# Optimization experiments

Measured on AMD Instinct MI355X. Metric: run time of the kernel, lower is better.

## Reference

```python
import jax, jax.numpy as jnp
import numpy as np

B, K = 16, 256
APP, DK, DG, NR = 768, 96, 96, 8


def setup_inputs() -> dict:
    key = jax.random.key(0)
    ks = jax.random.split(key, 10)
    sA = 1.0 / np.sqrt(APP)  # torch Linear default init scale
    sG = 1.0 / np.sqrt(DG)
    return {
        "f_a": jax.random.normal(ks[0], (B, K, APP), jnp.float32),
        "position_embedding": jax.random.uniform(ks[1], (B, K, K, DG), jnp.float32),
        "WG_w": jax.random.normal(ks[2], (NR, DG), jnp.float32) * sG,
        "WG_b": jnp.zeros((NR,), jnp.float32),
        "WK_w": jax.random.normal(ks[3], (NR, DK, APP), jnp.float32) * sA,
        "WK_b": jnp.zeros((NR, DK), jnp.float32),
        "WQ_w": jax.random.normal(ks[4], (NR, DK, APP), jnp.float32) * sA,
        "WQ_b": jnp.zeros((NR, DK), jnp.float32),
        "WV_w": jax.random.normal(ks[5], (NR, DK, APP), jnp.float32) * sA,
        "WV_b": jnp.zeros((NR, DK), jnp.float32),
    }


def reference(f_a, position_embedding, WG_w, WG_b, WK_w, WK_b, WQ_w, WQ_b, WV_w, WV_b):
    # geometric bias: [NR, B, K, K]
    w_g = jax.nn.relu(jnp.einsum('bmng,rg->rbmn', position_embedding, WG_w)
                      + WG_b[:, None, None, None])
    # projections: [NR, B, K, DK]
    w_k = jnp.einsum('bmd,rkd->rbmk', f_a, WK_w) + WK_b[:, None, None, :]
    w_q = jnp.einsum('bnd,rkd->rbnk', f_a, WQ_w) + WQ_b[:, None, None, :]
    w_v = jnp.einsum('bmd,rkd->rbmk', f_a, WV_w) + WV_b[:, None, None, :]
    # scaled dot: scores[r,b,m,n] = <k_m, q_n>/sqrt(DK)
    scores = jnp.einsum('rbmk,rbnk->rbmn', w_k, w_q) / jnp.sqrt(jnp.float32(DK))
    logits = jnp.log(jnp.clip(w_g, 1e-6)) + scores
    # softmax over m (the key index, torch dim=1 of [B,K,K])
    att = jax.nn.softmax(logits, axis=2)
    # out[r,b,n,k] = sum_m att[r,b,m,n] * v[r,b,m,k]
    out = jnp.einsum('rbmn,rbmk->rbnk', att, w_v)
    # concat units along feature dim -> [B, K, NR*DK], residual add
    out = out.transpose(1, 2, 0, 3).reshape(B, K, NR * DK)
    return out + f_a
```

## Files before the change

### kernel.cpp

```cpp
#include <hip/hip_runtime.h>
#include <hip/hip_bf16.h>

typedef __attribute__((ext_vector_type(8))) short s16x8;
typedef __attribute__((ext_vector_type(4))) float f32x4;
typedef unsigned short u16;
typedef unsigned int u32;

#define NB 16
#define NK 256
#define APP 768
#define DKK 96
#define NR 8
#define QSCALE 0.10206207261596575f

__device__ __forceinline__ u16 f2bf(float f) {
  union { float f; unsigned int u; } v; v.f = f;
  unsigned int x = v.u;
  x += 0x7fffu + ((x >> 16) & 1u);
  return (u16)(x >> 16);
}
__device__ __forceinline__ float bf2f(u16 h) {
  union { unsigned int u; float f; } v; v.u = ((unsigned int)h) << 16;
  return v.f;
}
__device__ __forceinline__ u32 cvtpk(float lo, float hi) {
  u32 r;
  asm("v_cvt_pk_bf16_f32 %0, %1, %2" : "=v"(r) : "v"(lo), "v"(hi));
  return r;
}
__device__ __forceinline__ float bflo(u32 pk) {
  union { u32 u; float f; } v; v.u = pk << 16; return v.f;
}
__device__ __forceinline__ float bfhi(u32 pk) {
  union { u32 u; float f; } v; v.u = pk & 0xffff0000u; return v.f;
}
__device__ __forceinline__ void gload_lds16(const void* g, void* l) {
  __builtin_amdgcn_global_load_lds(
      (const __attribute__((address_space(1))) unsigned int*)g,
      (__attribute__((address_space(3))) unsigned int*)l, 16, 0, 0);
}

__global__ __launch_bounds__(256) void conv_kernel(
    const float* __restrict__ fa,
    const float* __restrict__ WKw, const float* __restrict__ WQw,
    const float* __restrict__ WVw,
    u16* __restrict__ fab, u16* __restrict__ Wb)
{
  const int idx = blockIdx.x * 256 + threadIdx.x;
  const int faCh = NB * NK * APP / 8;
  const int wCh  = NR * DKK * APP / 8;
  const float* src; u16* dst;
  if (idx < faCh) {
    src = fa + (size_t)idx * 8;
    dst = fab + (size_t)idx * 8;
  } else {
    int o = idx - faCh;
    int a = o / wCh;
    int oo = o - a * wCh;
    const float* wsrc = a == 0 ? WKw : (a == 1 ? WQw : WVw);
    src = wsrc + (size_t)oo * 8;
    dst = Wb + (size_t)a * (NR * DKK * APP) + (size_t)oo * 8;
  }
  float4 v0 = *(const float4*)src;
  float4 v1 = *(const float4*)(src + 4);
  s16x8 ov = {(short)f2bf(v0.x),(short)f2bf(v0.y),(short)f2bf(v0.z),(short)f2bf(v0.w),
              (short)f2bf(v1.x),(short)f2bf(v1.y),(short)f2bf(v1.z),(short)f2bf(v1.w)};
  *(s16x8*)dst = ov;
}

__global__ __launch_bounds__(256) void proj_kernel(
    const u16* __restrict__ fab, const u16* __restrict__ Wb,
    const float* __restrict__ WKb, const float* __restrict__ WQb,
    const float* __restrict__ WVb,
    u16* __restrict__ wkF, u16* __restrict__ wqF, u16* __restrict__ wvF)
{
  __shared__ u16 As[128 * 64];
  __shared__ u16 Bs[128 * 64];
  const int t = threadIdx.x;
  const int lane = t & 63, w = t >> 6;
  const int c = lane & 15, g = lane >> 4;
  const int wr = w >> 1, wc = w & 1;
  const int m0 = blockIdx.x * 128;
  const int ct = blockIdx.y;
  const int c0 = ct * 128;

  f32x4 acc[4][4] = {};

  for (int k0 = 0; k0 < APP; k0 += 64) {
    __syncthreads();
    #pragma unroll
    for (int i = 0; i < 4; ++i) {
      int n = t + i * 256;
      int row = n >> 3, cg = n & 7;
      int scg = cg ^ (row & 7);
      gload_lds16(fab + (size_t)(m0 + row) * APP + k0 + scg * 8, As + n * 8);
      gload_lds16(Wb  + (size_t)(c0 + row) * APP + k0 + scg * 8, Bs + n * 8);
    }
    __syncthreads();
    #pragma unroll
    for (int kc = 0; kc < 2; ++kc) {
      s16x8 af[4], bfr[4];
      #pragma unroll
      for (int i = 0; i < 4; ++i) {
        int arow = wr * 64 + i * 16 + c;
        af[i]  = *(const s16x8*)(As + (((arow << 3) | ((kc * 4 + g) ^ (arow & 7))) << 3));
        int brow = wc * 64 + i * 16 + c;
        bfr[i] = *(const s16x8*)(Bs + (((brow << 3) | ((kc * 4 + g) ^ (brow & 7))) << 3));
      }
      #pragma unroll
      for (int mi = 0; mi < 4; ++mi)
        #pragma unroll
        for (int ni = 0; ni < 4; ++ni)
          acc[mi][ni] = __builtin_amdgcn_mfma_f32_16x16x32_bf16(af[mi], bfr[ni], acc[mi][ni], 0, 0, 0);
    }
  }

  const int arr = ct / 6;
  const int cw0 = c0 - arr * APP;
  const float* bp = arr == 0 ? WKb : (arr == 1 ? WQb : WVb);

  #pragma unroll
  for (int mi = 0; mi < 4; ++mi)
    #pragma unroll
    for (int ni = 0; ni < 4; ++ni) {
      int clw = cw0 + wc * 64 + ni * 16 + c;
      float bias = bp[clw];
      int rr = clw / DKK, kk = clw - rr * DKK;
      int mb = m0 + wr * 64 + mi * 16 + g * 4;
      int bi = mb >> 8, tt = mb & 255;
      size_t hb = (size_t)rr * NB + bi;
      if (arr == 2) {
        ushort4 pk4;
        pk4.x = f2bf(acc[mi][ni][0] + bias);
        pk4.y = f2bf(acc[mi][ni][1] + bias);
        pk4.z = f2bf(acc[mi][ni][2] + bias);
        pk4.w = f2bf(acc[mi][ni][3] + bias);
        *(ushort4*)&wvF[((hb * 32 + (tt >> 3)) * DKK + kk) * 8 + (tt & 7)] = pk4;
      } else {
        u16* op = arr == 0 ? wkF : wqF;
        size_t base = ((hb * 12 + (kk >> 3)) * NK) * 8 + (size_t)(kk & 7);
        #pragma unroll
        for (int e = 0; e < 4; ++e) {
          float val = acc[mi][ni][e] + bias;
          if (arr == 1) val *= QSCALE;
          op[base + (size_t)(tt + e) * 8] = f2bf(val);
        }
      }
    }
}

__global__ __launch_bounds__(256) void wg_kernel(
    const float* __restrict__ pos,
    const float* __restrict__ WGw, const float* __restrict__ WGb,
    u16* __restrict__ lb2)
{
  __shared__ u16 Th[128 * 104];
  __shared__ u16 Tl[128 * 104];
  const int t = threadIdx.x;
  const int lane = t & 63, w = t >> 6;
  const int c = lane & 15, g = lane >> 4;
  const size_t row0 = (size_t)blockIdx.x * 128;

  s16x8 bwh[3], bwl[3];
  #pragma unroll
  for (int kc = 0; kc < 3; ++kc) {
    const float* wp = WGw + (c & 7) * DKK + kc * 32 + g * 8;
    s16x8 hv, lv;
    #pragma unroll
    for (int j = 0; j < 4; ++j) {
      float x0 = wp[2 * j], x1 = wp[2 * j + 1];
      u32 h = cvtpk(x0, x1);
      u32 l = cvtpk(x0 - bflo(h), x1 - bfhi(h));
      hv[2 * j] = (short)(h & 0xffff); hv[2 * j + 1] = (short)(h >> 16);
      lv[2 * j] = (short)(l & 0xffff); lv[2 * j + 1] = (short)(l >> 16);
    }
    bwh[kc] = hv; bwl[kc] = lv;
  }
  const float bias = WGb[c & 7];

  #pragma unroll
  for (int i = 0; i < 6; ++i) {
    int q = t + i * 256;
    int row = q / 12, col8 = q - row * 12;
    const float* s = pos + row0 * DKK + (size_t)q * 8;
    float4 a = *(const float4*)s;
    float4 b = *(const float4*)(s + 4);
    uint4 ph, pl;
    ph.x = cvtpk(a.x, a.y); pl.x = cvtpk(a.x - bflo(ph.x), a.y - bfhi(ph.x));
    ph.y = cvtpk(a.z, a.w); pl.y = cvtpk(a.z - bflo(ph.y), a.w - bfhi(ph.y));
    ph.z = cvtpk(b.x, b.y); pl.z = cvtpk(b.x - bflo(ph.z), b.y - bfhi(ph.z));
    ph.w = cvtpk(b.z, b.w); pl.w = cvtpk(b.z - bflo(ph.w), b.w - bfhi(ph.w));
    *(uint4*)&Th[row * 104 + col8 * 8] = ph;
    *(uint4*)&Tl[row * 104 + col8 * 8] = pl;
  }
  __syncthreads();

  #pragma unroll
  for (int gi = 0; gi < 2; ++gi) {
    int rowl = w * 32 + gi * 16;
    f32x4 acc = {0.f, 0.f, 0.f, 0.f};
    #pragma unroll
    for (int kc = 0; kc < 3; ++kc) {
      s16x8 ah = *(const s16x8*)&Th[(rowl + c) * 104 + kc * 32 + g * 8];
      s16x8 al = *(const s16x8*)&Tl[(rowl + c) * 104 + kc * 32 + g * 8];
      acc = __builtin_amdgcn_mfma_f32_16x16x32_bf16(ah, bwh[kc], acc, 0, 0, 0);
      acc = __builtin_amdgcn_mfma_f32_16x16x32_bf16(ah, bwl[kc], acc, 0, 0, 0);
      acc = __builtin_amdgcn_mfma_f32_16x16x32_bf16(al, bwh[kc], acc, 0, 0, 0);
    }
    if (c < 8) {
      size_t base = (size_t)c * (NB * NK * NK) + row0 + rowl + g * 4;
      #pragma unroll
      for (int e = 0; e < 4; ++e) {
        float v = __logf(fmaxf(acc[e] + bias, 1e-6f));
        lb2[base + e] = f2bf(v);
      }
    }
  }
}

__global__ __launch_bounds__(256) void attn_kernel(
    const u16* __restrict__ wkF, const u16* __restrict__ wqF,
    const u16* __restrict__ wvF, const u16* __restrict__ lb2,
    const float* __restrict__ fa, float* __restrict__ out)
{
  __shared__ u16 Ps[4][16][40];
  const int t = threadIdx.x;
  const int w = t >> 6, lane = t & 63;
  const int c = lane & 15, g = lane >> 4;
  const int b = blockIdx.y, r = blockIdx.z;
  const int nb = blockIdx.x * 64 + w * 16;

  const size_t hb = (size_t)r * NB + b;
  const u16* Qb = wqF + hb * (12 * NK * 8);
  const u16* Kb = wkF + hb * (12 * NK * 8);
  const u16* Vb = wvF + hb * (32 * DKK * 8);
  const u16* Br = lb2 + hb * NK * NK + (size_t)c * NK + nb + g * 4;

  s16x8 qf[3];
  #pragma unroll
  for (int kc = 0; kc < 3; ++kc)
    qf[kc] = *(const s16x8*)(Qb + ((kc * 4 + g) * NK + nb + c) * 8);

  ushort4 bbr[16];
  #pragma unroll
  for (int mt = 0; mt < 16; ++mt)
    bbr[mt] = *(const ushort4*)(Br + (size_t)mt * 16 * NK);

  f32x4 S[16];
  #pragma unroll
  for (int mt = 0; mt < 16; ++mt) {
    f32x4 sa = {bf2f(bbr[mt].x), bf2f(bbr[mt].y), bf2f(bbr[mt].z), bf2f(bbr[mt].w)};
    #pragma unroll
    for (int kc = 0; kc < 3; ++kc) {
      s16x8 kf = *(const s16x8*)(Kb + ((kc * 4 + g) * NK + mt * 16 + c) * 8);
      sa = __builtin_amdgcn_mfma_f32_16x16x32_bf16(qf[kc], kf, sa, 0, 0, 0);
    }
    S[mt] = sa;
  }

  float rinv[4];
  #pragma unroll
  for (int e = 0; e < 4; ++e) {
    float mx = S[0][e];
    #pragma unroll
    for (int mt = 1; mt < 16; ++mt) mx = fmaxf(mx, S[mt][e]);
    mx = fmaxf(mx, __shfl_xor(mx, 1));
    mx = fmaxf(mx, __shfl_xor(mx, 2));
    mx = fmaxf(mx, __shfl_xor(mx, 4));
    mx = fmaxf(mx, __shfl_xor(mx, 8));
    float sm = 0.f;
    #pragma unroll
    for (int mt = 0; mt < 16; ++mt) {
      float p = __expf(S[mt][e] - mx);
      S[mt][e] = p;
      sm += p;
    }
    sm += __shfl_xor(sm, 1);
    sm += __shfl_xor(sm, 2);
    sm += __shfl_xor(sm, 4);
    sm += __shfl_xor(sm, 8);
    rinv[e] = 1.f / sm;
  }

  f32x4 o[6];
  #pragma unroll
  for (int ki = 0; ki < 6; ++ki) o[ki] = (f32x4){0.f, 0.f, 0.f, 0.f};

  #pragma unroll
  for (int mc = 0; mc < 8; ++mc) {
    #pragma unroll
    for (int e = 0; e < 4; ++e) {
      Ps[w][g * 4 + e][c]      = f2bf(S[2 * mc][e]);
      Ps[w][g * 4 + e][16 + c] = f2bf(S[2 * mc + 1][e]);
    }
    s16x8 pa = *(const s16x8*)&Ps[w][c][g * 8];
    #pragma unroll
    for (int ki = 0; ki < 6; ++ki) {
      s16x8 vf = *(const s16x8*)(Vb + ((mc * 4 + g) * DKK + ki * 16 + c) * 8);
      o[ki] = __builtin_amdgcn_mfma_f32_16x16x32_bf16(pa, vf, o[ki], 0, 0, 0);
    }
  }

  #pragma unroll
  for (int ki = 0; ki < 6; ++ki)
    #pragma unroll
    for (int e = 0; e < 4; ++e) {
      int n = nb + g * 4 + e;
      size_t adr = ((size_t)b * NK + n) * (NR * DKK) + r * DKK + ki * 16 + c;
      out[adr] = o[ki][e] * rinv[e] + fa[adr];
    }
}

extern "C" void kernel_launch(void* const* d_in, const int* in_sizes, int n_in,
                              void* d_out, int out_size, void* d_ws, size_t ws_size,
                              hipStream_t stream) {
  (void)in_sizes; (void)n_in; (void)out_size; (void)ws_size;
  const float* fa  = (const float*)d_in[0];
  const float* pos = (const float*)d_in[1];
  const float* WGw = (const float*)d_in[2];
  const float* WGb = (const float*)d_in[3];
  const float* WKw = (const float*)d_in[4];
  const float* WKb = (const float*)d_in[5];
  const float* WQw = (const float*)d_in[6];
  const float* WQb = (const float*)d_in[7];
  const float* WVw = (const float*)d_in[8];
  const float* WVb = (const float*)d_in[9];
  float* outp = (float*)d_out;

  const size_t faN = (size_t)NB * NK * APP;
  const size_t wN  = (size_t)3 * NR * DKK * APP;
  const size_t kqv = (size_t)NR * NB * NK * DKK;
  u16* fab = (u16*)d_ws;
  u16* Wb  = fab + faN;
  u16* wkF = Wb + wN;
  u16* wqF = wkF + kqv;
  u16* wvF = wqF + kqv;
  u16* lb2 = wvF + kqv;

  hipLaunchKernelGGL(conv_kernel, dim3(2400), dim3(256), 0, stream,
                     fa, WKw, WQw, WVw, fab, Wb);
  hipLaunchKernelGGL(proj_kernel, dim3(32, 18), dim3(256), 0, stream,
                     fab, Wb, WKb, WQb, WVb, wkF, wqF, wvF);
  hipLaunchKernelGGL(wg_kernel, dim3(8192), dim3(256), 0, stream,
                     pos, WGw, WGb, lb2);
  hipLaunchKernelGGL(attn_kernel, dim3(4, NB, NR), dim3(256), 0, stream,
                     wkF, wqF, wvF, lb2, fa, outp);
}
```

Measured before the change: 146.5 us.

## Fuse projection GEMM and geometric-bias kernels into one interleaved launch

Merges the QKV projection GEMM and the position-embedding bias kernel into one grid. Every 15th block runs a compute-heavy projection tile and the rest run memory-bound bias tiles, so the two workloads overlap on the CUs and one launch boundary is removed. The bias kernel's log output is also packed into a single 8-byte store per lane instead of four 2-byte stores. Shared memory per block is sized for the larger bias tile, which may reduce occupancy for the projection blocks.

```diff
diff --git a/kernel.cpp b/kernel.cpp
--- a/kernel.cpp
+++ b/kernel.cpp
@@ -68,151 +68,160 @@
   *(s16x8*)dst = ov;
 }
 
-__global__ __launch_bounds__(256) void proj_kernel(
+#define PROJ_BLKS 576
+#define WG_BLKS 8192
+
+__global__ __launch_bounds__(256) void fused_kernel(
     const u16* __restrict__ fab, const u16* __restrict__ Wb,
     const float* __restrict__ WKb, const float* __restrict__ WQb,
     const float* __restrict__ WVb,
-    u16* __restrict__ wkF, u16* __restrict__ wqF, u16* __restrict__ wvF)
-{
-  __shared__ u16 As[128 * 64];
-  __shared__ u16 Bs[128 * 64];
-  const int t = threadIdx.x;
-  const int lane = t & 63, w = t >> 6;
-  const int c = lane & 15, g = lane >> 4;
-  const int wr = w >> 1, wc = w & 1;
-  const int m0 = blockIdx.x * 128;
-  const int ct = blockIdx.y;
-  const int c0 = ct * 128;
-
-  f32x4 acc[4][4] = {};
-
-  for (int k0 = 0; k0 < APP; k0 += 64) {
-    __syncthreads();
-    #pragma unroll
-    for (int i = 0; i < 4; ++i) {
-      int n = t + i * 256;
-      int row = n >> 3, cg = n & 7;
-      int scg = cg ^ (row & 7);
-      gload_lds16(fab + (size_t)(m0 + row) * APP + k0 + scg * 8, As + n * 8);
-      gload_lds16(Wb  + (size_t)(c0 + row) * APP + k0 + scg * 8, Bs + n * 8);
-    }
-    __syncthreads();
-    #pragma unroll
-    for (int kc = 0; kc < 2; ++kc) {
-      s16x8 af[4], bfr[4];
-      #pragma unroll
-      for (int i = 0; i < 4; ++i) {
-        int arow = wr * 64 + i * 16 + c;
-        af[i]  = *(const s16x8*)(As + (((arow << 3) | ((kc * 4 + g) ^ (arow & 7))) << 3));
-        int brow = wc * 64 + i * 16 + c;
-        bfr[i] = *(const s16x8*)(Bs + (((brow << 3) | ((kc * 4 + g) ^ (brow & 7))) << 3));
-      }
-      #pragma unroll
-      for (int mi = 0; mi < 4; ++mi)
-        #pragma unroll
-        for (int ni = 0; ni < 4; ++ni)
-          acc[mi][ni] = __builtin_amdgcn_mfma_f32_16x16x32_bf16(af[mi], bfr[ni], acc[mi][ni], 0, 0, 0);
-    }
-  }
-
-  const int arr = ct / 6;
-  const int cw0 = c0 - arr * APP;
-  const float* bp = arr == 0 ? WKb : (arr == 1 ? WQb : WVb);
-
-  #pragma unroll
-  for (int mi = 0; mi < 4; ++mi)
-    #pragma unroll
-    for (int ni = 0; ni < 4; ++ni) {
-      int clw = cw0 + wc * 64 + ni * 16 + c;
-      float bias = bp[clw];
-      int rr = clw / DKK, kk = clw - rr * DKK;
-      int mb = m0 + wr * 64 + mi * 16 + g * 4;
-      int bi = mb >> 8, tt = mb & 255;
-      size_t hb = (size_t)rr * NB + bi;
-      if (arr == 2) {
-        ushort4 pk4;
-        pk4.x = f2bf(acc[mi][ni][0] + bias);
-        pk4.y = f2bf(acc[mi][ni][1] + bias);
-        pk4.z = f2bf(acc[mi][ni][2] + bias);
-        pk4.w = f2bf(acc[mi][ni][3] + bias);
-        *(ushort4*)&wvF[((hb * 32 + (tt >> 3)) * DKK + kk) * 8 + (tt & 7)] = pk4;
-      } else {
-        u16* op = arr == 0 ? wkF : wqF;
-        size_t base = ((hb * 12 + (kk >> 3)) * NK) * 8 + (size_t)(kk & 7);
-        #pragma unroll
-        for (int e = 0; e < 4; ++e) {
-          float val = acc[mi][ni][e] + bias;
-          if (arr == 1) val *= QSCALE;
-          op[base + (size_t)(tt + e) * 8] = f2bf(val);
-        }
-      }
-    }
-}
-
-__global__ __launch_bounds__(256) void wg_kernel(
+    u16* __restrict__ wkF, u16* __restrict__ wqF, u16* __restrict__ wvF,
     const float* __restrict__ pos,
     const float* __restrict__ WGw, const float* __restrict__ WGb,
     u16* __restrict__ lb2)
 {
-  __shared__ u16 Th[128 * 104];
-  __shared__ u16 Tl[128 * 104];
+  __shared__ u16 SH[26624];
   const int t = threadIdx.x;
   const int lane = t & 63, w = t >> 6;
   const int c = lane & 15, g = lane >> 4;
-  const size_t row0 = (size_t)blockIdx.x * 128;
-
-  s16x8 bwh[3], bwl[3];
-  #pragma unroll
-  for (int kc = 0; kc < 3; ++kc) {
-    const float* wp = WGw + (c & 7) * DKK + kc * 32 + g * 8;
-    s16x8 hv, lv;
-    #pragma unroll
-    for (int j = 0; j < 4; ++j) {
-      float x0 = wp[2 * j], x1 = wp[2 * j + 1];
-      u32 h = cvtpk(x0, x1);
-      u32 l = cvtpk(x0 - bflo(h), x1 - bfhi(h));
-      hv[2 * j] = (short)(h & 0xffff); hv[2 * j + 1] = (short)(h >> 16);
-      lv[2 * j] = (short)(l & 0xffff); lv[2 * j + 1] = (short)(l >> 16);
-    }
-    bwh[kc] = hv; bwl[kc] = lv;
-  }
-  const float bias = WGb[c & 7];
-
-  #pragma unroll
-  for (int i = 0; i < 6; ++i) {
-    int q = t + i * 256;
-    int row = q / 12, col8 = q - row * 12;
-    const float* s = pos + row0 * DKK + (size_t)q * 8;
-    float4 a = *(const float4*)s;
-    float4 b = *(const float4*)(s + 4);
-    uint4 ph, pl;
-    ph.x = cvtpk(a.x, a.y); pl.x = cvtpk(a.x - bflo(ph.x), a.y - bfhi(ph.x));
-    ph.y = cvtpk(a.z, a.w); pl.y = cvtpk(a.z - bflo(ph.y), a.w - bfhi(ph.y));
-    ph.z = cvtpk(b.x, b.y); pl.z = cvtpk(b.x - bflo(ph.z), b.y - bfhi(ph.z));
-    ph.w = cvtpk(b.z, b.w); pl.w = cvtpk(b.z - bflo(ph.w), b.w - bfhi(ph.w));
-    *(uint4*)&Th[row * 104 + col8 * 8] = ph;
-    *(uint4*)&Tl[row * 104 + col8 * 8] = pl;
-  }
-  __syncthreads();
-
-  #pragma unroll
-  for (int gi = 0; gi < 2; ++gi) {
-    int rowl = w * 32 + gi * 16;
-    f32x4 acc = {0.f, 0.f, 0.f, 0.f};
+  const int bid = blockIdx.x;
+  const int q = bid / 15, rph = bid - q * 15;
+
+  if (rph == 0 && q < PROJ_BLKS) {
+    u16* As = SH;
+    u16* Bs = SH + 8192;
+    const int pb = q;
+    const int wr = w >> 1, wc = w & 1;
+    const int m0 = (pb & 31) * 128;
+    const int ct = pb >> 5;
+    const int c0 = ct * 128;
+
+    f32x4 acc[4][4] = {};
+
+    for (int k0 = 0; k0 < APP; k0 += 64) {
+      __syncthreads();
+      #pragma unroll
+      for (int i = 0; i < 4; ++i) {
+        int n = t + i * 256;
+        int row = n >> 3, cg = n & 7;
+        int scg = cg ^ (row & 7);
+        gload_lds16(fab + (size_t)(m0 + row) * APP + k0 + scg * 8, As + n * 8);
+        gload_lds16(Wb  + (size_t)(c0 + row) * APP + k0 + scg * 8, Bs + n * 8);
+      }
+      __syncthreads();
+      #pragma unroll
+      for (int kc = 0; kc < 2; ++kc) {
+        s16x8 af[4], bfr[4];
+        #pragma unroll
+        for (int i = 0; i < 4; ++i) {
+          int arow = wr * 64 + i * 16 + c;
+          af[i]  = *(const s16x8*)(As + (((arow << 3) | ((kc * 4 + g) ^ (arow & 7))) << 3));
+          int brow = wc * 64 + i * 16 + c;
+          bfr[i] = *(const s16x8*)(Bs + (((brow << 3) | ((kc * 4 + g) ^ (brow & 7))) << 3));
+        }
+        #pragma unroll
+        for (int mi = 0; mi < 4; ++mi)
+          #pragma unroll
+          for (int ni = 0; ni < 4; ++ni)
+            acc[mi][ni] = __builtin_amdgcn_mfma_f32_16x16x32_bf16(af[mi], bfr[ni], acc[mi][ni], 0, 0, 0);
+      }
+    }
+
+    const int arr = ct / 6;
+    const int cw0 = c0 - arr * APP;
+    const float* bp = arr == 0 ? WKb : (arr == 1 ? WQb : WVb);
+
+    #pragma unroll
+    for (int mi = 0; mi < 4; ++mi)
+      #pragma unroll
+      for (int ni = 0; ni < 4; ++ni) {
+        int clw = cw0 + wc * 64 + ni * 16 + c;
+        float bias = bp[clw];
+        int rr = clw / DKK, kk = clw - rr * DKK;
+        int mb = m0 + wr * 64 + mi * 16 + g * 4;
+        int bi = mb >> 8, tt = mb & 255;
+        size_t hb = (size_t)rr * NB + bi;
+        if (arr == 2) {
+          ushort4 pk4;
+          pk4.x = f2bf(acc[mi][ni][0] + bias);
+          pk4.y = f2bf(acc[mi][ni][1] + bias);
+          pk4.z = f2bf(acc[mi][ni][2] + bias);
+          pk4.w = f2bf(acc[mi][ni][3] + bias);
+          *(ushort4*)&wvF[((hb * 32 + (tt >> 3)) * DKK + kk) * 8 + (tt & 7)] = pk4;
+        } else {
+          u16* op = arr == 0 ? wkF : wqF;
+          size_t base = ((hb * 12 + (kk >> 3)) * NK) * 8 + (size_t)(kk & 7);
+          #pragma unroll
+          for (int e = 0; e < 4; ++e) {
+            float val = acc[mi][ni][e] + bias;
+            if (arr == 1) val *= QSCALE;
+            op[base + (size_t)(tt + e) * 8] = f2bf(val);
+          }
+        }
+      }
+  } else {
+    const int nbefore = (q >= PROJ_BLKS) ? PROJ_BLKS : (q + (rph > 0 ? 1 : 0));
+    const int wgid = bid - nbefore;
+    u16* Th = SH;
+    u16* Tl = SH + 13312;
+    const size_t row0 = (size_t)wgid * 128;
+
+    s16x8 bwh[3], bwl[3];
     #pragma unroll
     for (int kc = 0; kc < 3; ++kc) {
-      s16x8 ah = *(const s16x8*)&Th[(rowl + c) * 104 + kc * 32 + g * 8];
-      s16x8 al = *(const s16x8*)&Tl[(rowl + c) * 104 + kc * 32 + g * 8];
-      acc = __builtin_amdgcn_mfma_f32_16x16x32_bf16(ah, bwh[kc], acc, 0, 0, 0);
-      acc = __builtin_amdgcn_mfma_f32_16x16x32_bf16(ah, bwl[kc], acc, 0, 0, 0);
-      acc = __builtin_amdgcn_mfma_f32_16x16x32_bf16(al, bwh[kc], acc, 0, 0, 0);
-    }
-    if (c < 8) {
-      size_t base = (size_t)c * (NB * NK * NK) + row0 + rowl + g * 4;
-      #pragma unroll
-      for (int e = 0; e < 4; ++e) {
-        float v = __logf(fmaxf(acc[e] + bias, 1e-6f));
-        lb2[base + e] = f2bf(v);
+      const float* wp = WGw + (c & 7) * DKK + kc * 32 + g * 8;
+      s16x8 hv, lv;
+      #pragma unroll
+      for (int j = 0; j < 4; ++j) {
+        float x0 = wp[2 * j], x1 = wp[2 * j + 1];
+        u32 h = cvtpk(x0, x1);
+        u32 l = cvtpk(x0 - bflo(h), x1 - bfhi(h));
+        hv[2 * j] = (short)(h & 0xffff); hv[2 * j + 1] = (short)(h >> 16);
+        lv[2 * j] = (short)(l & 0xffff); lv[2 * j + 1] = (short)(l >> 16);
+      }
+      bwh[kc] = hv; bwl[kc] = lv;
+    }
+    const float bias = WGb[c & 7];
+
+    #pragma unroll
+    for (int i = 0; i < 6; ++i) {
+      int qq = t + i * 256;
+      int row = qq / 12, col8 = qq - row * 12;
+      const float* s = pos + row0 * DKK + (size_t)qq * 8;
+      float4 a = *(const float4*)s;
+      float4 b = *(const float4*)(s + 4);
+      uint4 ph, pl;
+      ph.x = cvtpk(a.x, a.y); pl.x = cvtpk(a.x - bflo(ph.x), a.y - bfhi(ph.x));
+      ph.y = cvtpk(a.z, a.w); pl.y = cvtpk(a.z - bflo(ph.y), a.w - bfhi(ph.y));
+      ph.z = cvtpk(b.x, b.y); pl.z = cvtpk(b.x - bflo(ph.z), b.y - bfhi(ph.z));
+      ph.w = cvtpk(b.z, b.w); pl.w = cvtpk(b.z - bflo(ph.w), b.w - bfhi(ph.w));
+      *(uint4*)&Th[row * 104 + col8 * 8] = ph;
+      *(uint4*)&Tl[row * 104 + col8 * 8] = pl;
+    }
+    __syncthreads();
+
+    #pragma unroll
+    for (int gi = 0; gi < 2; ++gi) {
+      int rowl = w * 32 + gi * 16;
+      f32x4 acc = {0.f, 0.f, 0.f, 0.f};
+      #pragma unroll
+      for (int kc = 0; kc < 3; ++kc) {
+        s16x8 ah = *(const s16x8*)&Th[(rowl + c) * 104 + kc * 32 + g * 8];
+        s16x8 al = *(const s16x8*)&Tl[(rowl + c) * 104 + kc * 32 + g * 8];
+        acc = __builtin_amdgcn_mfma_f32_16x16x32_bf16(ah, bwh[kc], acc, 0, 0, 0);
+        acc = __builtin_amdgcn_mfma_f32_16x16x32_bf16(ah, bwl[kc], acc, 0, 0, 0);
+        acc = __builtin_amdgcn_mfma_f32_16x16x32_bf16(al, bwh[kc], acc, 0, 0, 0);
+      }
+      if (c < 8) {
+        size_t base = (size_t)c * (NB * NK * NK) + row0 + rowl + g * 4;
+        float v0 = __logf(fmaxf(acc[0] + bias, 1e-6f));
+        float v1 = __logf(fmaxf(acc[1] + bias, 1e-6f));
+        float v2 = __logf(fmaxf(acc[2] + bias, 1e-6f));
+        float v3 = __logf(fmaxf(acc[3] + bias, 1e-6f));
+        uint2 pk;
+        pk.x = cvtpk(v0, v1);
+        pk.y = cvtpk(v2, v3);
+        *(uint2*)(lb2 + base) = pk;
       }
     }
   }
@@ -339,10 +348,8 @@
 
   hipLaunchKernelGGL(conv_kernel, dim3(2400), dim3(256), 0, stream,
                      fa, WKw, WQw, WVw, fab, Wb);
-  hipLaunchKernelGGL(proj_kernel, dim3(32, 18), dim3(256), 0, stream,
-                     fab, Wb, WKb, WQb, WVb, wkF, wqF, wvF);
-  hipLaunchKernelGGL(wg_kernel, dim3(8192), dim3(256), 0, stream,
-                     pos, WGw, WGb, lb2);
+  hipLaunchKernelGGL(fused_kernel, dim3(PROJ_BLKS + WG_BLKS), dim3(256), 0, stream,
+                     fab, Wb, WKb, WQb, WVb, wkF, wqF, wvF, pos, WGw, WGb, lb2);
   hipLaunchKernelGGL(attn_kernel, dim3(4, NB, NR), dim3(256), 0, stream,
                      wkF, wqF, wvF, lb2, fa, outp);
 }
```

Measured after the change: 137.4 us. 1.07x faster.
